# Kernel tuning notes

Hardware: AMD Instinct MI355X
Metric: run time of the kernel (lower is better)

Reference implementation:

```python
import jax, jax.numpy as jnp
import numpy as np

N_NODES = 100000
N_EDGES = 1600000
IN_DIM = 128
HID = 64
CONV2_OUT = 8
GLOBAL_DIM = 24
OUT_DIM = 1
NUM_GRAPHS = 64
NEG_SLOPE = 0.01


def setup_inputs() -> dict:
    key = jax.random.key(0)
    ks = jax.random.split(key, 12)
    x = jax.random.normal(ks[0], (N_NODES, IN_DIM), dtype=jnp.float32)
    edge_index = jax.random.randint(ks[1], (2, N_EDGES), 0, N_NODES, dtype=jnp.int32)
    batch = jnp.sort(jax.random.randint(ks[2], (N_NODES,), 0, NUM_GRAPHS, dtype=jnp.int32))
    global_features = jax.random.normal(ks[3], (NUM_GRAPHS, GLOBAL_DIM), dtype=jnp.float32)
    # GCNConv weights (glorot-ish scale) and Linear weights
    W1 = jax.random.normal(ks[4], (IN_DIM, HID), dtype=jnp.float32) / np.sqrt(IN_DIM)
    b1 = jnp.zeros((HID,), dtype=jnp.float32)
    W2 = jax.random.normal(ks[5], (HID, CONV2_OUT), dtype=jnp.float32) / np.sqrt(HID)
    b2 = jnp.zeros((CONV2_OUT,), dtype=jnp.float32)
    fcW1 = jax.random.normal(ks[6], (GLOBAL_DIM + CONV2_OUT, 16), dtype=jnp.float32) / np.sqrt(GLOBAL_DIM + CONV2_OUT)
    fcb1 = jnp.zeros((16,), dtype=jnp.float32)
    fcW2 = jax.random.normal(ks[7], (16, OUT_DIM), dtype=jnp.float32) / np.sqrt(16)
    fcb2 = jnp.zeros((OUT_DIM,), dtype=jnp.float32)
    return {"x": x, "edge_index": edge_index, "batch": batch,
            "global_features": global_features,
            "W1": W1, "b1": b1, "W2": W2, "b2": b2,
            "fcW1": fcW1, "fcb1": fcb1, "fcW2": fcW2, "fcb2": fcb2}


def gcn_conv(x, src, dst, W, b):
    """PyG GCNConv: add self-loops, sym-normalize, aggregate x@W from src->dst."""
    n = x.shape[0]
    h = x @ W  # [N, F_out]
    loop = jnp.arange(n, dtype=src.dtype)
    src2 = jnp.concatenate([src, loop])
    dst2 = jnp.concatenate([dst, loop])
    deg = jax.ops.segment_sum(jnp.ones_like(dst2, dtype=h.dtype), dst2, num_segments=n)
    dinv = jnp.where(deg > 0, jax.lax.rsqrt(deg), 0.0)
    norm = dinv[src2] * dinv[dst2]  # [E+N]
    msg = h[src2] * norm[:, None]   # edge gather (dominant traffic)
    out = jax.ops.segment_sum(msg, dst2, num_segments=n)
    return out + b


def reference(x, edge_index, batch, global_features, W1, b1, W2, b2, fcW1, fcb1, fcW2, fcb2):
    src, dst = edge_index[0], edge_index[1]
    h = jax.nn.leaky_relu(gcn_conv(x, src, dst, W1, b1), NEG_SLOPE)
    h = jax.nn.leaky_relu(gcn_conv(h, src, dst, W2, b2), NEG_SLOPE)
    # global mean pool over graphs
    sums = jax.ops.segment_sum(h, batch, num_segments=NUM_GRAPHS)
    cnts = jax.ops.segment_sum(jnp.ones((h.shape[0],), h.dtype), batch, num_segments=NUM_GRAPHS)
    pool = sums / jnp.maximum(cnts, 1.0)[:, None]
    z = jnp.concatenate([pool, global_features], axis=1)
    z = jax.nn.leaky_relu(z @ fcW1 + fcb1, NEG_SLOPE)
    z = jax.nn.leaky_relu(z @ fcW2 + fcb2, NEG_SLOPE)
    return z
```

## Files before the change

kernel.cpp:

```cpp
#include <hip/hip_runtime.h>

constexpr int N_NODES = 100000;
constexpr int N_EDGES = 1600000;
constexpr int IN_DIM  = 128;
constexpr int HID     = 64;
constexpr int C2      = 8;
constexpr int GDIM    = 24;
constexpr int NG      = 64;
constexpr int NREP    = 8;
constexpr float SLOPE = 0.01f;
constexpr int NB_SCAN = (N_NODES + 255) / 256;

__device__ __forceinline__ float lrelu(float v) { return v > 0.f ? v : SLOPE * v; }

__device__ __forceinline__ float bflo(unsigned int u) { return __uint_as_float(u << 16); }
__device__ __forceinline__ float bfhi(unsigned int u) { return __uint_as_float(u & 0xffff0000u); }
__device__ __forceinline__ unsigned short f2bf(float f) {
    unsigned int i = __float_as_uint(f);
    unsigned int r = (i + 0x7fffu + ((i >> 16) & 1u)) >> 16;
    return (unsigned short)r;
}

__global__ void k_rank(const int* __restrict__ dst, int* __restrict__ cnt,
                       int* __restrict__ rnk) {
    int t = blockIdx.x * 256 + threadIdx.x;
    int* c = cnt + (size_t)(blockIdx.x & (NREP - 1)) * N_NODES;
    if (t < N_EDGES / 4) {
        int4 d = ((const int4*)dst)[t];
        int4 r;
        r.x = atomicAdd(&c[d.x], 1);
        r.y = atomicAdd(&c[d.y], 1);
        r.z = atomicAdd(&c[d.z], 1);
        r.w = atomicAdd(&c[d.w], 1);
        ((int4*)rnk)[t] = r;
    }
}

__global__ void k_scan1(const int* __restrict__ cnt, int* __restrict__ deg,
                        int* __restrict__ rowptr, int* __restrict__ bsum,
                        float* __restrict__ dinv) {
    __shared__ int s[256];
    int tid = threadIdx.x;
    int i = blockIdx.x * 256 + tid;
    int v = 0;
    if (i < N_NODES) {
#pragma unroll
        for (int r = 0; r < NREP; ++r) v += cnt[(size_t)r * N_NODES + i];
        deg[i] = v;
        dinv[i] = rsqrtf((float)(v + 1));
    }
    s[tid] = v;
    __syncthreads();
    for (int off = 1; off < 256; off <<= 1) {
        int t = (tid >= off) ? s[tid - off] : 0;
        __syncthreads();
        s[tid] += t;
        __syncthreads();
    }
    if (i < N_NODES) rowptr[i] = s[tid] - v;
    if (tid == 255) bsum[blockIdx.x] = s[255];
}

__global__ void k_scan2(const int* __restrict__ bsum, int* __restrict__ bsumx) {
    __shared__ int s[512];
    int tid = threadIdx.x;
    int v = (tid < NB_SCAN) ? bsum[tid] : 0;
    s[tid] = v;
    __syncthreads();
    for (int off = 1; off < 512; off <<= 1) {
        int t = (tid >= off) ? s[tid - off] : 0;
        __syncthreads();
        s[tid] += t;
        __syncthreads();
    }
    if (tid < NB_SCAN) bsumx[tid] = s[tid] - v;
}

__global__ void k_ofs(int* __restrict__ cnt, const int* __restrict__ rowptr,
                      const int* __restrict__ bsumx) {
    int i = blockIdx.x * 256 + threadIdx.x;
    if (i < N_NODES) {
        int g = rowptr[i] + bsumx[i >> 8];
#pragma unroll
        for (int r = 0; r < NREP; ++r) {
            int c = cnt[(size_t)r * N_NODES + i];
            cnt[(size_t)r * N_NODES + i] = g;
            g += c;
        }
    }
}

__global__ void k_place(const int* __restrict__ src, const int* __restrict__ dst,
                        const int* __restrict__ rnk, const int* __restrict__ cnt,
                        int* __restrict__ eidx) {
    int t = blockIdx.x * 256 + threadIdx.x;
    const int* ofs = cnt + (size_t)(blockIdx.x & (NREP - 1)) * N_NODES;
    if (t < N_EDGES / 4) {
        int4 d = ((const int4*)dst)[t];
        int4 r = ((const int4*)rnk)[t];
        int4 s = ((const int4*)src)[t];
        eidx[ofs[d.x] + r.x] = s.x;
        eidx[ofs[d.y] + r.y] = s.y;
        eidx[ofs[d.z] + r.z] = s.z;
        eidx[ofs[d.w] + r.w] = s.w;
    }
}

__global__ __launch_bounds__(256) void k_gemm1(const float* __restrict__ x,
                                               const float* __restrict__ W1,
                                               const float* __restrict__ dinv,
                                               unsigned short* __restrict__ hs1) {
    __shared__ float sW[IN_DIM * HID];
    __shared__ float sX[32][IN_DIM];
    int node0 = blockIdx.x * 32;
    for (int t = threadIdx.x; t < IN_DIM * HID / 4; t += 256)
        ((float4*)sW)[t] = ((const float4*)W1)[t];
    for (int t = threadIdx.x; t < 32 * IN_DIM / 4; t += 256) {
        int r = t >> 5, c4 = t & 31;
        ((float4*)&sX[r][0])[c4] = ((const float4*)(x + (size_t)(node0 + r) * IN_DIM))[c4];
    }
    __syncthreads();
    int col = threadIdx.x & 63;
    int nb  = (threadIdx.x >> 6) * 8;
    float acc[8] = {0.f, 0.f, 0.f, 0.f, 0.f, 0.f, 0.f, 0.f};
    for (int k4 = 0; k4 < IN_DIM; k4 += 4) {
        float w0 = sW[(k4 + 0) * HID + col];
        float w1 = sW[(k4 + 1) * HID + col];
        float w2 = sW[(k4 + 2) * HID + col];
        float w3 = sW[(k4 + 3) * HID + col];
#pragma unroll
        for (int j = 0; j < 8; ++j) {
            float4 xv = *((const float4*)&sX[nb + j][k4]);
            acc[j] += xv.x * w0 + xv.y * w1 + xv.z * w2 + xv.w * w3;
        }
    }
#pragma unroll
    for (int j = 0; j < 8; ++j) {
        int n = node0 + nb + j;
        hs1[(size_t)n * HID + col] = f2bf(acc[j] * dinv[n]);
    }
}

__global__ __launch_bounds__(256) void k_agg1(const int* __restrict__ rowptr,
                                              const int* __restrict__ bsumx,
                                              const int* __restrict__ deg,
                                              const int* __restrict__ eidx,
                                              const unsigned short* __restrict__ hs1,
                                              const float* __restrict__ dinv,
                                              const float* __restrict__ b1,
                                              const float* __restrict__ W2,
                                              float* __restrict__ hs2) {
    int lane = threadIdx.x & 63;
    int q    = lane & 7;
    int slot = lane >> 3;
    float w2f[8];
#pragma unroll
    for (int i = 0; i < 8; ++i) w2f[i] = W2[(8 * q + i) * C2 + slot];
    float4 bb0 = ((const float4*)b1)[2 * q];
    float4 bb1 = ((const float4*)b1)[2 * q + 1];
    float bv[8] = {bb0.x, bb0.y, bb0.z, bb0.w, bb1.x, bb1.y, bb1.z, bb1.w};
    int node_base = blockIdx.x * 16 + (threadIdx.x >> 6) * 4;

    for (int nn = 0; nn < 4; ++nn) {
        int node  = node_base + nn;
        int start = rowptr[node] + bsumx[node >> 8];
        int cnt   = deg[node];
        uint4 hv = ((const uint4*)(hs1 + (size_t)node * HID))[q];
        float acc[8] = {0.f, 0.f, 0.f, 0.f, 0.f, 0.f, 0.f, 0.f};
        for (int base = 0; base < cnt; base += 64) {
            int idx = (base + lane < cnt) ? eidx[start + base + lane] : 0;
            int lim = min(64, cnt - base);
            int trips = (lim + 15) >> 4;
            for (int t = 0; t < trips; ++t) {
                int k0 = slot + t * 16;
                int k1 = k0 + 8;
                int s0 = __shfl(idx, k0);
                int s1 = __shfl(idx, k1 & 63);
                uint4 v0 = ((const uint4*)(hs1 + (size_t)s0 * HID))[q];
                uint4 v1 = ((const uint4*)(hs1 + (size_t)s1 * HID))[q];
                if (k0 >= lim) { v0.x = 0; v0.y = 0; v0.z = 0; v0.w = 0; }
                if (k1 >= lim) { v1.x = 0; v1.y = 0; v1.z = 0; v1.w = 0; }
                acc[0] += bflo(v0.x); acc[1] += bfhi(v0.x);
                acc[2] += bflo(v0.y); acc[3] += bfhi(v0.y);
                acc[4] += bflo(v0.z); acc[5] += bfhi(v0.z);
                acc[6] += bflo(v0.w); acc[7] += bfhi(v0.w);
                acc[0] += bflo(v1.x); acc[1] += bfhi(v1.x);
                acc[2] += bflo(v1.y); acc[3] += bfhi(v1.y);
                acc[4] += bflo(v1.z); acc[5] += bfhi(v1.z);
                acc[6] += bflo(v1.w); acc[7] += bfhi(v1.w);
            }
        }
#pragma unroll
        for (int m = 8; m < 64; m <<= 1)
#pragma unroll
            for (int i = 0; i < 8; ++i) acc[i] += __shfl_xor(acc[i], m);
        float self[8] = {bflo(hv.x), bfhi(hv.x), bflo(hv.y), bfhi(hv.y),
                         bflo(hv.z), bfhi(hv.z), bflo(hv.w), bfhi(hv.w)};
        float di = dinv[node];
        float p = 0.f;
#pragma unroll
        for (int i = 0; i < 8; ++i) {
            float y = lrelu(di * (acc[i] + self[i]) + bv[i]);
            p += y * w2f[i];
        }
#pragma unroll
        for (int m = 1; m < 8; m <<= 1) p += __shfl_xor(p, m);
        if (q == 0) hs2[(size_t)node * C2 + slot] = p * di;
    }
}

__global__ __launch_bounds__(256) void k_agg2(const int* __restrict__ rowptr,
                                              const int* __restrict__ bsumx,
                                              const int* __restrict__ deg,
                                              const int* __restrict__ eidx,
                                              const float* __restrict__ hs2,
                                              const float* __restrict__ dinv,
                                              const float* __restrict__ b2,
                                              float* __restrict__ y2) {
    int lane = threadIdx.x & 63;
    int q    = lane & 1;
    int slot = lane >> 1;
    int node_base = blockIdx.x * 16 + (threadIdx.x >> 6) * 4;

    for (int nn = 0; nn < 4; ++nn) {
        int node  = node_base + nn;
        int start = rowptr[node] + bsumx[node >> 8];
        int cnt   = deg[node];
        float4 acc = make_float4(0.f, 0.f, 0.f, 0.f);
        for (int base = 0; base < cnt; base += 64) {
            int idx = (base + lane < cnt) ? eidx[start + base + lane] : 0;
            int lim = min(64, cnt - base);
            int s0 = __shfl(idx, slot);
            int s1 = __shfl(idx, slot + 32);
            float4 v0 = ((const float4*)(hs2 + (size_t)s0 * C2))[q];
            float4 v1 = ((const float4*)(hs2 + (size_t)s1 * C2))[q];
            if (slot >= lim)      { v0.x = 0.f; v0.y = 0.f; v0.z = 0.f; v0.w = 0.f; }
            if (slot + 32 >= lim) { v1.x = 0.f; v1.y = 0.f; v1.z = 0.f; v1.w = 0.f; }
            acc.x += v0.x + v1.x; acc.y += v0.y + v1.y;
            acc.z += v0.z + v1.z; acc.w += v0.w + v1.w;
        }
        for (int m = 2; m < 64; m <<= 1) {
            acc.x += __shfl_xor(acc.x, m); acc.y += __shfl_xor(acc.y, m);
            acc.z += __shfl_xor(acc.z, m); acc.w += __shfl_xor(acc.w, m);
        }
        if (slot == 0) {
            float4 h = ((const float4*)(hs2 + (size_t)node * C2))[q];
            float di = dinv[node];
            const float* bb = b2 + q * 4;
            float4 r;
            r.x = lrelu(di * (acc.x + h.x) + bb[0]);
            r.y = lrelu(di * (acc.y + h.y) + bb[1]);
            r.z = lrelu(di * (acc.z + h.z) + bb[2]);
            r.w = lrelu(di * (acc.w + h.w) + bb[3]);
            ((float4*)(y2 + (size_t)node * C2))[q] = r;
        }
    }
}

__device__ __forceinline__ int lower_bound(const int* __restrict__ b, int n, int v) {
    int lo = 0, hi = n;
    while (lo < hi) {
        int m = (lo + hi) >> 1;
        if (b[m] < v) lo = m + 1; else hi = m;
    }
    return lo;
}

__global__ __launch_bounds__(256) void k_pool(const float* __restrict__ y2,
                                              const int* __restrict__ batch,
                                              const float* __restrict__ gfeat,
                                              const float* __restrict__ fcW1,
                                              const float* __restrict__ fcb1,
                                              const float* __restrict__ fcW2,
                                              const float* __restrict__ fcb2,
                                              float* __restrict__ out) {
    __shared__ float s[256];
    int g   = blockIdx.x;
    int tid = threadIdx.x;
    int start = lower_bound(batch, N_NODES, g);
    int end   = lower_bound(batch, N_NODES, g + 1);
    int col = tid & 7;
    float local = 0.f;
    for (int n = start + (tid >> 3); n < end; n += 32)
        local += y2[(size_t)n * C2 + col];
    s[tid] = local;
    __syncthreads();
    for (int off = 128; off >= 8; off >>= 1) {
        if (tid < off) s[tid] += s[tid + off];
        __syncthreads();
    }
    if (tid == 0) {
        float cnt = fmaxf((float)(end - start), 1.f);
        float z[C2 + GDIM];
        for (int c = 0; c < C2; ++c) z[c] = s[c] / cnt;
        for (int c = 0; c < GDIM; ++c) z[C2 + c] = gfeat[g * GDIM + c];
        float acc2 = fcb2[0];
        for (int j = 0; j < 16; ++j) {
            float acc = fcb1[j];
            for (int c = 0; c < C2 + GDIM; ++c) acc += z[c] * fcW1[c * 16 + j];
            acc2 += lrelu(acc) * fcW2[j];
        }
        out[g] = lrelu(acc2);
    }
}

extern "C" void kernel_launch(void* const* d_in, const int* in_sizes, int n_in,
                              void* d_out, int out_size, void* d_ws, size_t ws_size,
                              hipStream_t stream) {
    const float* x     = (const float*)d_in[0];
    const int*   ei    = (const int*)d_in[1];
    const int*   batch = (const int*)d_in[2];
    const float* gfeat = (const float*)d_in[3];
    const float* W1    = (const float*)d_in[4];
    const float* b1    = (const float*)d_in[5];
    const float* W2    = (const float*)d_in[6];
    const float* b2    = (const float*)d_in[7];
    const float* fcW1  = (const float*)d_in[8];
    const float* fcb1  = (const float*)d_in[9];
    const float* fcW2  = (const float*)d_in[10];
    const float* fcb2  = (const float*)d_in[11];
    const int* src = ei;
    const int* dst = ei + N_EDGES;

    char* ws = (char*)d_ws;
    size_t off = 0;
    auto alloc = [&](size_t bytes) -> void* {
        void* p = ws + off;
        off = (off + bytes + 255) & ~(size_t)255;
        return p;
    };
    int*   cnt    = (int*)  alloc((size_t)NREP * N_NODES * 4);
    int*   deg    = (int*)  alloc((size_t)N_NODES * 4);
    float* dinv   = (float*)alloc((size_t)N_NODES * 4);
    int*   rowptr = (int*)  alloc((size_t)N_NODES * 4);
    int*   bsum   = (int*)  alloc(512 * 4);
    int*   bsumx  = (int*)  alloc(512 * 4);
    int*   rnk    = (int*)  alloc((size_t)N_EDGES * 4);
    int*   eidx   = (int*)  alloc((size_t)N_EDGES * 4);
    unsigned short* hs1 = (unsigned short*)alloc((size_t)N_NODES * HID * 2);
    float* hs2    = (float*)alloc((size_t)N_NODES * C2 * 4);
    float* y2     = (float*)alloc((size_t)N_NODES * C2 * 4);

    hipMemsetAsync(cnt, 0, (size_t)NREP * N_NODES * 4, stream);

    k_rank <<<(N_EDGES / 4 + 255) / 256, 256, 0, stream>>>(dst, cnt, rnk);
    k_scan1<<<NB_SCAN, 256, 0, stream>>>(cnt, deg, rowptr, bsum, dinv);
    k_scan2<<<1, 512, 0, stream>>>(bsum, bsumx);
    k_ofs  <<<NB_SCAN, 256, 0, stream>>>(cnt, rowptr, bsumx);
    k_place<<<(N_EDGES / 4 + 255) / 256, 256, 0, stream>>>(src, dst, rnk, cnt, eidx);

    k_gemm1<<<N_NODES / 32, 256, 0, stream>>>(x, W1, dinv, hs1);
    k_agg1 <<<N_NODES / 16, 256, 0, stream>>>(rowptr, bsumx, deg, eidx, hs1, dinv, b1, W2, hs2);
    k_agg2 <<<N_NODES / 16, 256, 0, stream>>>(rowptr, bsumx, deg, eidx, hs2, dinv, b2, y2);
    k_pool <<<NG, 256, 0, stream>>>(y2, batch, gfeat, fcW1, fcb1, fcW2, fcb2, (float*)d_out);
}
```

Measured before the change: 260.8 us.

## Co-schedule rank with GEMM and placement with bf16 scaling in merged launches

The edge-rank atomics and the x@W1 GEMM now share one launch. The GEMM writes unscaled fp32 results to a temporary buffer. The edge placement and the dinv scaling plus bf16 packing now share a second launch. This lets independent memory-bound and compute work overlap and removes kernel boundaries, at the cost of an extra fp32 write and read of the N×64 intermediate. The aggregation kernels are also changed to process 8 nodes per wave with half as many blocks, and hs2/y2 alias into the raw buffer.

Result: no change. 260.2 us (-0.2%).

```diff
diff --git a/kernel.cpp b/kernel.cpp
--- a/kernel.cpp
+++ b/kernel.cpp
@@ -10,30 +10,67 @@
 constexpr int NREP    = 8;
 constexpr float SLOPE = 0.01f;
 constexpr int NB_SCAN = (N_NODES + 255) / 256;
+constexpr int RANK_BLOCKS  = (N_EDGES / 4 + 255) / 256;
+constexpr int GEMMF_BLOCKS = N_NODES / 16;
+constexpr int PLACE_BLOCKS = RANK_BLOCKS;
+constexpr int SCALE_BLOCKS = N_NODES * HID / 8 / 256;
 
 __device__ __forceinline__ float lrelu(float v) { return v > 0.f ? v : SLOPE * v; }
 
 __device__ __forceinline__ float bflo(unsigned int u) { return __uint_as_float(u << 16); }
 __device__ __forceinline__ float bfhi(unsigned int u) { return __uint_as_float(u & 0xffff0000u); }
-__device__ __forceinline__ unsigned short f2bf(float f) {
+__device__ __forceinline__ unsigned int f2bf_u(float f) {
     unsigned int i = __float_as_uint(f);
-    unsigned int r = (i + 0x7fffu + ((i >> 16) & 1u)) >> 16;
-    return (unsigned short)r;
-}
-
-__global__ void k_rank(const int* __restrict__ dst, int* __restrict__ cnt,
-                       int* __restrict__ rnk) {
-    int t = blockIdx.x * 256 + threadIdx.x;
-    int* c = cnt + (size_t)(blockIdx.x & (NREP - 1)) * N_NODES;
-    if (t < N_EDGES / 4) {
-        int4 d = ((const int4*)dst)[t];
-        int4 r;
-        r.x = atomicAdd(&c[d.x], 1);
-        r.y = atomicAdd(&c[d.y], 1);
-        r.z = atomicAdd(&c[d.z], 1);
-        r.w = atomicAdd(&c[d.w], 1);
-        ((int4*)rnk)[t] = r;
-    }
+    return (i + 0x7fffu + ((i >> 16) & 1u)) >> 16;
+}
+
+__global__ __launch_bounds__(256) void k_front(const float* __restrict__ x,
+                                               const float* __restrict__ W1,
+                                               const int* __restrict__ dst,
+                                               int* __restrict__ cnt,
+                                               int* __restrict__ rnk,
+                                               float* __restrict__ raw) {
+    __shared__ float sW[IN_DIM * HID];
+    __shared__ float sX[16][IN_DIM];
+    if (blockIdx.x < RANK_BLOCKS) {
+        int t = blockIdx.x * 256 + threadIdx.x;
+        int* c = cnt + (size_t)(blockIdx.x & (NREP - 1)) * N_NODES;
+        if (t < N_EDGES / 4) {
+            int4 d = ((const int4*)dst)[t];
+            int4 r;
+            r.x = atomicAdd(&c[d.x], 1);
+            r.y = atomicAdd(&c[d.y], 1);
+            r.z = atomicAdd(&c[d.z], 1);
+            r.w = atomicAdd(&c[d.w], 1);
+            ((int4*)rnk)[t] = r;
+        }
+        return;
+    }
+    int node0 = (blockIdx.x - RANK_BLOCKS) * 16;
+    for (int t = threadIdx.x; t < IN_DIM * HID / 4; t += 256)
+        ((float4*)sW)[t] = ((const float4*)W1)[t];
+    for (int t = threadIdx.x; t < 16 * IN_DIM / 4; t += 256) {
+        int r = t >> 5, c4 = t & 31;
+        ((float4*)&sX[r][0])[c4] = ((const float4*)(x + (size_t)(node0 + r) * IN_DIM))[c4];
+    }
+    __syncthreads();
+    int col = threadIdx.x & 63;
+    int nb  = (threadIdx.x >> 6) * 4;
+    float acc[4] = {0.f, 0.f, 0.f, 0.f};
+    for (int k4 = 0; k4 < IN_DIM; k4 += 4) {
+        float w0 = sW[(k4 + 0) * HID + col];
+        float w1 = sW[(k4 + 1) * HID + col];
+        float w2 = sW[(k4 + 2) * HID + col];
+        float w3 = sW[(k4 + 3) * HID + col];
+#pragma unroll
+        for (int j = 0; j < 4; ++j) {
+            float4 xv = *((const float4*)&sX[nb + j][k4]);
+            acc[j] += xv.x * w0 + xv.y * w1 + xv.z * w2 + xv.w * w3;
+        }
+    }
+#pragma unroll
+    for (int j = 0; j < 4; ++j)
+        raw[(size_t)(node0 + nb + j) * HID + col] = acc[j];
 }
 
 __global__ void k_scan1(const int* __restrict__ cnt, int* __restrict__ deg,
@@ -90,55 +127,39 @@
     }
 }
 
-__global__ void k_place(const int* __restrict__ src, const int* __restrict__ dst,
-                        const int* __restrict__ rnk, const int* __restrict__ cnt,
-                        int* __restrict__ eidx) {
-    int t = blockIdx.x * 256 + threadIdx.x;
-    const int* ofs = cnt + (size_t)(blockIdx.x & (NREP - 1)) * N_NODES;
-    if (t < N_EDGES / 4) {
-        int4 d = ((const int4*)dst)[t];
-        int4 r = ((const int4*)rnk)[t];
-        int4 s = ((const int4*)src)[t];
-        eidx[ofs[d.x] + r.x] = s.x;
-        eidx[ofs[d.y] + r.y] = s.y;
-        eidx[ofs[d.z] + r.z] = s.z;
-        eidx[ofs[d.w] + r.w] = s.w;
-    }
-}
-
-__global__ __launch_bounds__(256) void k_gemm1(const float* __restrict__ x,
-                                               const float* __restrict__ W1,
-                                               const float* __restrict__ dinv,
-                                               unsigned short* __restrict__ hs1) {
-    __shared__ float sW[IN_DIM * HID];
-    __shared__ float sX[32][IN_DIM];
-    int node0 = blockIdx.x * 32;
-    for (int t = threadIdx.x; t < IN_DIM * HID / 4; t += 256)
-        ((float4*)sW)[t] = ((const float4*)W1)[t];
-    for (int t = threadIdx.x; t < 32 * IN_DIM / 4; t += 256) {
-        int r = t >> 5, c4 = t & 31;
-        ((float4*)&sX[r][0])[c4] = ((const float4*)(x + (size_t)(node0 + r) * IN_DIM))[c4];
-    }
-    __syncthreads();
-    int col = threadIdx.x & 63;
-    int nb  = (threadIdx.x >> 6) * 8;
-    float acc[8] = {0.f, 0.f, 0.f, 0.f, 0.f, 0.f, 0.f, 0.f};
-    for (int k4 = 0; k4 < IN_DIM; k4 += 4) {
-        float w0 = sW[(k4 + 0) * HID + col];
-        float w1 = sW[(k4 + 1) * HID + col];
-        float w2 = sW[(k4 + 2) * HID + col];
-        float w3 = sW[(k4 + 3) * HID + col];
-#pragma unroll
-        for (int j = 0; j < 8; ++j) {
-            float4 xv = *((const float4*)&sX[nb + j][k4]);
-            acc[j] += xv.x * w0 + xv.y * w1 + xv.z * w2 + xv.w * w3;
-        }
-    }
-#pragma unroll
-    for (int j = 0; j < 8; ++j) {
-        int n = node0 + nb + j;
-        hs1[(size_t)n * HID + col] = f2bf(acc[j] * dinv[n]);
-    }
+__global__ __launch_bounds__(256) void k_mid(const int* __restrict__ src,
+                                             const int* __restrict__ dst,
+                                             const int* __restrict__ rnk,
+                                             const int* __restrict__ cnt,
+                                             int* __restrict__ eidx,
+                                             const float* __restrict__ raw,
+                                             const float* __restrict__ dinv,
+                                             unsigned short* __restrict__ hs1) {
+    if (blockIdx.x < PLACE_BLOCKS) {
+        int t = blockIdx.x * 256 + threadIdx.x;
+        const int* ofs = cnt + (size_t)(blockIdx.x & (NREP - 1)) * N_NODES;
+        if (t < N_EDGES / 4) {
+            int4 d = ((const int4*)dst)[t];
+            int4 r = ((const int4*)rnk)[t];
+            int4 s = ((const int4*)src)[t];
+            eidx[ofs[d.x] + r.x] = s.x;
+            eidx[ofs[d.y] + r.y] = s.y;
+            eidx[ofs[d.z] + r.z] = s.z;
+            eidx[ofs[d.w] + r.w] = s.w;
+        }
+        return;
+    }
+    int t = (blockIdx.x - PLACE_BLOCKS) * 256 + threadIdx.x;
+    int node = t >> 3;
+    float di = dinv[node];
+    float4 a = ((const float4*)raw)[2 * t];
+    float4 b = ((const float4*)raw)[2 * t + 1];
+    uint4 o;
+    o.x = f2bf_u(a.x * di) | (f2bf_u(a.y * di) << 16);
+    o.y = f2bf_u(a.z * di) | (f2bf_u(a.w * di) << 16);
+    o.z = f2bf_u(b.x * di) | (f2bf_u(b.y * di) << 16);
+    o.w = f2bf_u(b.z * di) | (f2bf_u(b.w * di) << 16);
+    ((uint4*)hs1)[t] = o;
 }
 
 __global__ __launch_bounds__(256) void k_agg1(const int* __restrict__ rowptr,
@@ -159,9 +180,9 @@
     float4 bb0 = ((const float4*)b1)[2 * q];
     float4 bb1 = ((const float4*)b1)[2 * q + 1];
     float bv[8] = {bb0.x, bb0.y, bb0.z, bb0.w, bb1.x, bb1.y, bb1.z, bb1.w};
-    int node_base = blockIdx.x * 16 + (threadIdx.x >> 6) * 4;
-
-    for (int nn = 0; nn < 4; ++nn) {
+    int node_base = blockIdx.x * 32 + (threadIdx.x >> 6) * 8;
+
+    for (int nn = 0; nn < 8; ++nn) {
         int node  = node_base + nn;
         int start = rowptr[node] + bsumx[node >> 8];
         int cnt   = deg[node];
@@ -220,9 +241,9 @@
     int lane = threadIdx.x & 63;
     int q    = lane & 1;
     int slot = lane >> 1;
-    int node_base = blockIdx.x * 16 + (threadIdx.x >> 6) * 4;
-
-    for (int nn = 0; nn < 4; ++nn) {
+    int node_base = blockIdx.x * 32 + (threadIdx.x >> 6) * 8;
+
+    for (int nn = 0; nn < 8; ++nn) {
         int node  = node_base + nn;
         int start = rowptr[node] + bsumx[node >> 8];
         int cnt   = deg[node];
@@ -338,19 +359,19 @@
     int*   rnk    = (int*)  alloc((size_t)N_EDGES * 4);
     int*   eidx   = (int*)  alloc((size_t)N_EDGES * 4);
     unsigned short* hs1 = (unsigned short*)alloc((size_t)N_NODES * HID * 2);
-    float* hs2    = (float*)alloc((size_t)N_NODES * C2 * 4);
-    float* y2     = (float*)alloc((size_t)N_NODES * C2 * 4);
+    float* raw    = (float*)alloc((size_t)N_NODES * HID * 4);
+    float* hs2 = raw;
+    float* y2  = raw + (size_t)N_NODES * C2;
 
     hipMemsetAsync(cnt, 0, (size_t)NREP * N_NODES * 4, stream);
 
-    k_rank <<<(N_EDGES / 4 + 255) / 256, 256, 0, stream>>>(dst, cnt, rnk);
+    k_front<<<RANK_BLOCKS + GEMMF_BLOCKS, 256, 0, stream>>>(x, W1, dst, cnt, rnk, raw);
     k_scan1<<<NB_SCAN, 256, 0, stream>>>(cnt, deg, rowptr, bsum, dinv);
     k_scan2<<<1, 512, 0, stream>>>(bsum, bsumx);
     k_ofs  <<<NB_SCAN, 256, 0, stream>>>(cnt, rowptr, bsumx);
-    k_place<<<(N_EDGES / 4 + 255) / 256, 256, 0, stream>>>(src, dst, rnk, cnt, eidx);
-
-    k_gemm1<<<N_NODES / 32, 256, 0, stream>>>(x, W1, dinv, hs1);
-    k_agg1 <<<N_NODES / 16, 256, 0, stream>>>(rowptr, bsumx, deg, eidx, hs1, dinv, b1, W2, hs2);
-    k_agg2 <<<N_NODES / 16, 256, 0, stream>>>(rowptr, bsumx, deg, eidx, hs2, dinv, b2, y2);
+    k_mid  <<<PLACE_BLOCKS + SCALE_BLOCKS, 256, 0, stream>>>(src, dst, rnk, cnt, eidx,
+                                                             raw, dinv, hs1);
+    k_agg1 <<<N_NODES / 32, 256, 0, stream>>>(rowptr, bsumx, deg, eidx, hs1, dinv, b1, W2, hs2);
+    k_agg2 <<<N_NODES / 32, 256, 0, stream>>>(rowptr, bsumx, deg, eidx, hs2, dinv, b2, y2);
     k_pool <<<NG, 256, 0, stream>>>(y2, batch, gfeat, fcW1, fcb1, fcW2, fcb2, (float*)d_out);
 }
```
